# Performance work log

Measured on AMD Instinct MI355X. Metric: run time of the kernel, lower is better.

The kernel has to match this reference:

```python
import jax, jax.numpy as jnp
import numpy as np

N, F, H, F_ = 8192, 256, 2, 64
NEG_MASK = -1e10
LEAKY_SLOPE = 0.2


def setup_inputs() -> dict:
    key = jax.random.key(0)
    k0, k1, k2, k3 = jax.random.split(key, 4)
    X = jax.random.normal(k0, (N, F), jnp.float32)
    A = (jax.random.uniform(k1, (N, N)) < 0.01).astype(jnp.float32)
    A = jnp.maximum(A, jnp.eye(N, dtype=jnp.float32))
    W = jax.random.normal(k2, (H, F, F_), jnp.float32) * (1.0 / np.sqrt(F))
    b = jnp.zeros((H, F_), jnp.float32)
    a = jax.random.normal(k3, (H, F_), jnp.float32) * 0.1
    return {"X": X, "A": A, "W": W, "b": b, "a": a}


def reference(X, A, W, b, a):
    # per-head projected features: [H, N, F_]
    feats = jnp.einsum('nf,hfo->hno', X, W)
    # score[h,i,j] = sum_o feats[h,i,o] * feats[h,j,o] * a[h,o]
    # (identical math to Dot(axes=-1)([X_0*X_1, a^T]) without the [N,N,F_] tensor)
    scores = jnp.einsum('hno,hmo->hnm', feats * a[:, None, :], feats)
    scores = jax.nn.leaky_relu(scores, negative_slope=LEAKY_SLOPE)
    scores = scores + NEG_MASK * (1.0 - A)  # adjacency mask (broadcast over heads)
    attn = jax.nn.softmax(scores, axis=-1)  # [H, N, N]
    # dropout_rate=0 -> identity at inference
    out = jnp.einsum('hnm,hmo->hno', attn, feats) + b[:, None, :]  # [H, N, F_]
    out = jnp.transpose(out, (1, 0, 2)).reshape(X.shape[0], H * F_)  # concat heads
    return jax.nn.relu(out)
```

## Files before the change

kernel.cpp:

```cpp
#include <hip/hip_runtime.h>

#define NN 8192
#define FIN 256
#define FO 64
#define CAP 192

typedef float nf4 __attribute__((ext_vector_type(4)));
typedef unsigned long long ull;

__global__ __launch_bounds__(256) void feats_kernel(
    const float* __restrict__ X,
    const float* __restrict__ W,
    float* __restrict__ feats)
{
    __shared__ float Ws[128*FO];
    __shared__ float Xs[32*132];
    const int h = blockIdx.y;
    const int row0 = blockIdx.x * 32;
    const int t = threadIdx.x;
    const int rg = t >> 4;
    const int c0 = (t & 15) << 2;
    float acc0[4] = {0.f,0.f,0.f,0.f};
    float acc1[4] = {0.f,0.f,0.f,0.f};

    for (int kp = 0; kp < 2; ++kp){
        const int kb = kp * 128;
        const float* Wh = W + h*FIN*FO + kb*FO;
        #pragma unroll
        for (int it=0; it<8; ++it){
            int flat = (it*256 + t)*4;
            *(float4*)&Ws[flat] = *(const float4*)&Wh[flat];
        }
        #pragma unroll
        for (int it=0; it<4; ++it){
            int flat = (it*256 + t)*4;
            int r = flat >> 7, f0 = flat & 127;
            *(float4*)&Xs[r*132 + f0] = *(const float4*)&X[(size_t)(row0+r)*FIN + kb + f0];
        }
        __syncthreads();
        const float* xp0 = &Xs[(rg*2+0)*132];
        const float* xp1 = &Xs[(rg*2+1)*132];
        #pragma unroll 4
        for (int k=0; k<128; ++k){
            float x0 = xp0[k], x1 = xp1[k];
            float4 w4 = *(const float4*)&Ws[k*FO + c0];
            acc0[0]=fmaf(x0,w4.x,acc0[0]); acc0[1]=fmaf(x0,w4.y,acc0[1]);
            acc0[2]=fmaf(x0,w4.z,acc0[2]); acc0[3]=fmaf(x0,w4.w,acc0[3]);
            acc1[0]=fmaf(x1,w4.x,acc1[0]); acc1[1]=fmaf(x1,w4.y,acc1[1]);
            acc1[2]=fmaf(x1,w4.z,acc1[2]); acc1[3]=fmaf(x1,w4.w,acc1[3]);
        }
        __syncthreads();
    }
    float* o0 = feats + (size_t)(row0 + rg*2 + 0)*128 + h*FO + c0;
    float* o1 = feats + (size_t)(row0 + rg*2 + 1)*128 + h*FO + c0;
    *(float4*)o0 = make_float4(acc0[0],acc0[1],acc0[2],acc0[3]);
    *(float4*)o1 = make_float4(acc1[0],acc1[1],acc1[2],acc1[3]);
}

__global__ __launch_bounds__(256) void gat_kernel(
    const float* __restrict__ A,
    const float* __restrict__ feats,
    const float* __restrict__ av,
    const float* __restrict__ bv,
    float* __restrict__ out)
{
    __shared__ int   jsh[4][CAP];
    __shared__ float psh[4][2][CAP];
    __shared__ float qsh[4][128];

    const int t = threadIdx.x, w = t >> 6, l = t & 63;
    const int i = blockIdx.x*4 + w;
    const int h  = l & 1,  m  = l >> 1;
    const int ha = l >> 5, oa = (l & 31) * 2;
    const ull ltmask = (1ull << l) - 1ull;

    qsh[w][l]      = feats[(size_t)i*128 + l]      * av[l];
    qsh[w][64 + l] = feats[(size_t)i*128 + 64 + l] * av[64 + l];

    const nf4* Ar = (const nf4*)(A + (size_t)i*NN);
    int cnt = 0;
    #pragma unroll
    for (int s=0; s<4; ++s){
        nf4 v[8];
        #pragma unroll
        for (int r=0; r<8; ++r) v[r] = __builtin_nontemporal_load(&Ar[(s*8+r)*64 + l]);
        #pragma unroll
        for (int r=0; r<8; ++r){
            ull m0 = __ballot(v[r].x != 0.0f);
            ull m1 = __ballot(v[r].y != 0.0f);
            ull m2 = __ballot(v[r].z != 0.0f);
            ull m3 = __ballot(v[r].w != 0.0f);
            const int colb = ((s*8+r)*64 + l)*4;
            if ((m0>>l)&1){ int p = cnt + __popcll(m0 & ltmask); if (p<CAP) jsh[w][p] = colb;   }
            cnt += __popcll(m0);
            if ((m1>>l)&1){ int p = cnt + __popcll(m1 & ltmask); if (p<CAP) jsh[w][p] = colb+1; }
            cnt += __popcll(m1);
            if ((m2>>l)&1){ int p = cnt + __popcll(m2 & ltmask); if (p<CAP) jsh[w][p] = colb+2; }
            cnt += __popcll(m2);
            if ((m3>>l)&1){ int p = cnt + __popcll(m3 & ltmask); if (p<CAP) jsh[w][p] = colb+3; }
            cnt += __popcll(m3);
        }
    }
    const int n = min(cnt, CAP);
    __threadfence_block();

    float sr[6];
    const int nr = (n + 31) >> 5;
    float mx = -1e30f;
    const float4* qh = (const float4*)&qsh[w][h*64];
    for (int r=0; r<nr; ++r){
        int k = r*32 + m;
        bool valid = k < n;
        int j = valid ? jsh[w][k] : i;
        const float4* fj = (const float4*)&feats[(size_t)j*128 + h*64];
        float s = 0.f;
        #pragma unroll
        for (int u=0; u<16; ++u){
            float4 f = fj[u], qq = qh[u];
            s += f.x*qq.x + f.y*qq.y + f.z*qq.z + f.w*qq.w;
        }
        s = (s >= 0.f) ? s : 0.2f*s;
        if (!valid) s = -1e30f;
        sr[r] = s;
        mx = fmaxf(mx, s);
    }
    #pragma unroll
    for (int off=2; off<64; off<<=1) mx = fmaxf(mx, __shfl_xor(mx, off, 64));
    float sum = 0.f;
    for (int r=0; r<nr; ++r){ float p = __expf(sr[r] - mx); sr[r] = p; sum += p; }
    #pragma unroll
    for (int off=2; off<64; off<<=1) sum += __shfl_xor(sum, off, 64);
    const float inv = 1.0f / sum;
    for (int r=0; r<nr; ++r){
        int k = r*32 + m;
        if (k < n) psh[w][h][k] = sr[r] * inv;
    }
    __threadfence_block();

    const float* ph = psh[w][ha];
    const int fo = ha*64 + oa;
    float2 acc = make_float2(0.f, 0.f);
    int k = 0;
    for (; k+3 < n; k += 4){
        int j0 = jsh[w][k], j1 = jsh[w][k+1], j2 = jsh[w][k+2], j3 = jsh[w][k+3];
        float2 f0 = *(const float2*)&feats[(size_t)j0*128 + fo];
        float2 f1 = *(const float2*)&feats[(size_t)j1*128 + fo];
        float2 f2 = *(const float2*)&feats[(size_t)j2*128 + fo];
        float2 f3 = *(const float2*)&feats[(size_t)j3*128 + fo];
        float p0 = ph[k], p1 = ph[k+1], p2 = ph[k+2], p3 = ph[k+3];
        acc.x = fmaf(p0, f0.x, acc.x); acc.y = fmaf(p0, f0.y, acc.y);
        acc.x = fmaf(p1, f1.x, acc.x); acc.y = fmaf(p1, f1.y, acc.y);
        acc.x = fmaf(p2, f2.x, acc.x); acc.y = fmaf(p2, f2.y, acc.y);
        acc.x = fmaf(p3, f3.x, acc.x); acc.y = fmaf(p3, f3.y, acc.y);
    }
    for (; k < n; ++k){
        int j = jsh[w][k];
        float2 f = *(const float2*)&feats[(size_t)j*128 + fo];
        float p = ph[k];
        acc.x = fmaf(p, f.x, acc.x); acc.y = fmaf(p, f.y, acc.y);
    }
    float2 bb = *(const float2*)&bv[fo];
    float2 o2 = make_float2(fmaxf(acc.x + bb.x, 0.f), fmaxf(acc.y + bb.y, 0.f));
    *(float2*)&out[(size_t)i*128 + fo] = o2;
}

extern "C" void kernel_launch(void* const* d_in, const int* in_sizes, int n_in,
                              void* d_out, int out_size, void* d_ws, size_t ws_size,
                              hipStream_t stream) {
    const float* X = (const float*)d_in[0];
    const float* A = (const float*)d_in[1];
    const float* W = (const float*)d_in[2];
    const float* b = (const float*)d_in[3];
    const float* a = (const float*)d_in[4];
    float* out = (float*)d_out;

    float* feats = (float*)d_ws;

    feats_kernel<<<dim3(NN/32, 2), 256, 0, stream>>>(X, W, feats);
    gat_kernel  <<<dim3(NN/4),     256, 0, stream>>>(A, feats, a, b, out);
}
```

Measured before the change: 429.0 us.

## Double-buffer adjacency row loads and coalesce score gathers across lanes

The adjacency scan now runs eight stages of four float4 loads each, issuing the next stage's loads before the current stage is compacted. This software-pipelines the A-row stream, which dominates memory traffic, and uses fewer live registers than the previous eight-load batches. The score computation is also restructured: 16 lanes read one neighbor's 64-float head slice with coalesced float4 loads and reduce the dot product with shuffles, instead of each lane reading a whole row serially. Scores go through shared memory for a separate softmax pass, which adds a shared-memory round trip and extra shuffle reductions.

```diff
diff --git a/kernel.cpp b/kernel.cpp
--- a/kernel.cpp
+++ b/kernel.cpp
@@ -65,84 +65,101 @@
     float* __restrict__ out)
 {
     __shared__ int   jsh[4][CAP];
-    __shared__ float psh[4][2][CAP];
-    __shared__ float qsh[4][128];
+    __shared__ float sh0[4][CAP], sh1[4][CAP];
 
     const int t = threadIdx.x, w = t >> 6, l = t & 63;
     const int i = blockIdx.x*4 + w;
-    const int h  = l & 1,  m  = l >> 1;
-    const int ha = l >> 5, oa = (l & 31) * 2;
+    const int l32 = l & 31, g = l >> 5;
     const ull ltmask = (1ull << l) - 1ull;
 
-    qsh[w][l]      = feats[(size_t)i*128 + l]      * av[l];
-    qsh[w][64 + l] = feats[(size_t)i*128 + 64 + l] * av[64 + l];
+    int*   jw  = jsh[w];
+    float* sw0 = sh0[w];
+    float* sw1 = sh1[w];
+
+    float4 qa = *(const float4*)&av[l32*4];
+    float4 qf = *(const float4*)&feats[(size_t)i*128 + l32*4];
+    const float4 q4 = make_float4(qf.x*qa.x, qf.y*qa.y, qf.z*qa.z, qf.w*qa.w);
 
     const nf4* Ar = (const nf4*)(A + (size_t)i*NN);
+    nf4 cur[4], nxt[4];
+    #pragma unroll
+    for (int r=0; r<4; ++r) cur[r] = __builtin_nontemporal_load(&Ar[r*64 + l]);
     int cnt = 0;
-    #pragma unroll
-    for (int s=0; s<4; ++s){
-        nf4 v[8];
+    for (int s=0; s<8; ++s){
+        if (s < 7){
+            #pragma unroll
+            for (int r=0; r<4; ++r) nxt[r] = __builtin_nontemporal_load(&Ar[((s+1)*4+r)*64 + l]);
+        }
         #pragma unroll
-        for (int r=0; r<8; ++r) v[r] = __builtin_nontemporal_load(&Ar[(s*8+r)*64 + l]);
-        #pragma unroll
-        for (int r=0; r<8; ++r){
-            ull m0 = __ballot(v[r].x != 0.0f);
-            ull m1 = __ballot(v[r].y != 0.0f);
-            ull m2 = __ballot(v[r].z != 0.0f);
-            ull m3 = __ballot(v[r].w != 0.0f);
-            const int colb = ((s*8+r)*64 + l)*4;
-            if ((m0>>l)&1){ int p = cnt + __popcll(m0 & ltmask); if (p<CAP) jsh[w][p] = colb;   }
+        for (int r=0; r<4; ++r){
+            const int colb = ((s*4+r)*64 + l)*4;
+            bool n0 = (cur[r].x != 0.0f), n1 = (cur[r].y != 0.0f);
+            bool n2 = (cur[r].z != 0.0f), n3 = (cur[r].w != 0.0f);
+            ull m0 = __ballot(n0), m1 = __ballot(n1), m2 = __ballot(n2), m3 = __ballot(n3);
+            if (n0){ int p = cnt + __popcll(m0 & ltmask); if (p<CAP) jw[p] = colb;   }
             cnt += __popcll(m0);
-            if ((m1>>l)&1){ int p = cnt + __popcll(m1 & ltmask); if (p<CAP) jsh[w][p] = colb+1; }
+            if (n1){ int p = cnt + __popcll(m1 & ltmask); if (p<CAP) jw[p] = colb+1; }
             cnt += __popcll(m1);
-            if ((m2>>l)&1){ int p = cnt + __popcll(m2 & ltmask); if (p<CAP) jsh[w][p] = colb+2; }
+            if (n2){ int p = cnt + __popcll(m2 & ltmask); if (p<CAP) jw[p] = colb+2; }
             cnt += __popcll(m2);
-            if ((m3>>l)&1){ int p = cnt + __popcll(m3 & ltmask); if (p<CAP) jsh[w][p] = colb+3; }
+            if (n3){ int p = cnt + __popcll(m3 & ltmask); if (p<CAP) jw[p] = colb+3; }
             cnt += __popcll(m3);
         }
+        #pragma unroll
+        for (int r=0; r<4; ++r) cur[r] = nxt[r];
     }
     const int n = min(cnt, CAP);
     __threadfence_block();
 
-    float sr[6];
-    const int nr = (n + 31) >> 5;
-    float mx = -1e30f;
-    const float4* qh = (const float4*)&qsh[w][h*64];
-    for (int r=0; r<nr; ++r){
-        int k = r*32 + m;
-        bool valid = k < n;
-        int j = valid ? jsh[w][k] : i;
-        const float4* fj = (const float4*)&feats[(size_t)j*128 + h*64];
-        float s = 0.f;
+    for (int kb=0; kb<n; kb+=8){
+        float4 f[4];
         #pragma unroll
-        for (int u=0; u<16; ++u){
-            float4 f = fj[u], qq = qh[u];
-            s += f.x*qq.x + f.y*qq.y + f.z*qq.z + f.w*qq.w;
+        for (int u=0; u<4; ++u){
+            int k = kb + 2*u + g;
+            int j = (k < n) ? jw[k] : i;
+            f[u] = *(const float4*)&feats[(size_t)j*128 + l32*4];
         }
-        s = (s >= 0.f) ? s : 0.2f*s;
-        if (!valid) s = -1e30f;
-        sr[r] = s;
-        mx = fmaxf(mx, s);
-    }
-    #pragma unroll
-    for (int off=2; off<64; off<<=1) mx = fmaxf(mx, __shfl_xor(mx, off, 64));
-    float sum = 0.f;
-    for (int r=0; r<nr; ++r){ float p = __expf(sr[r] - mx); sr[r] = p; sum += p; }
-    #pragma unroll
-    for (int off=2; off<64; off<<=1) sum += __shfl_xor(sum, off, 64);
-    const float inv = 1.0f / sum;
-    for (int r=0; r<nr; ++r){
-        int k = r*32 + m;
-        if (k < n) psh[w][h][k] = sr[r] * inv;
+        #pragma unroll
+        for (int u=0; u<4; ++u){
+            int k = kb + 2*u + g;
+            float d = f[u].x*q4.x + f[u].y*q4.y + f[u].z*q4.z + f[u].w*q4.w;
+            d += __shfl_xor(d, 1, 64);
+            d += __shfl_xor(d, 2, 64);
+            d += __shfl_xor(d, 4, 64);
+            d += __shfl_xor(d, 8, 64);
+            d = (d >= 0.f) ? d : 0.2f*d;
+            if (k < n){
+                if (l32 == 0)  sw0[k] = d;
+                if (l32 == 16) sw1[k] = d;
+            }
+        }
     }
     __threadfence_block();
 
-    const float* ph = psh[w][ha];
-    const int fo = ha*64 + oa;
+    {
+        float* ss = g ? sw1 : sw0;
+        float m = -1e30f;
+        for (int k=l32; k<n; k+=32) m = fmaxf(m, ss[k]);
+        #pragma unroll
+        for (int off=16; off; off>>=1) m = fmaxf(m, __shfl_xor(m, off, 64));
+        float sum = 0.f;
+        float pr[6];
+        int nr = 0;
+        for (int k=l32; k<n; k+=32){ float p = __expf(ss[k]-m); pr[nr++] = p; sum += p; }
+        #pragma unroll
+        for (int off=16; off; off>>=1) sum += __shfl_xor(sum, off, 64);
+        const float inv = 1.0f / sum;
+        nr = 0;
+        for (int k=l32; k<n; k+=32) ss[k] = pr[nr++] * inv;
+    }
+    __threadfence_block();
+
+    const float* ph = g ? sw1 : sw0;
+    const int fo = g*64 + l32*2;
     float2 acc = make_float2(0.f, 0.f);
     int k = 0;
     for (; k+3 < n; k += 4){
-        int j0 = jsh[w][k], j1 = jsh[w][k+1], j2 = jsh[w][k+2], j3 = jsh[w][k+3];
+        int j0 = jw[k], j1 = jw[k+1], j2 = jw[k+2], j3 = jw[k+3];
         float2 f0 = *(const float2*)&feats[(size_t)j0*128 + fo];
         float2 f1 = *(const float2*)&feats[(size_t)j1*128 + fo];
         float2 f2 = *(const float2*)&feats[(size_t)j2*128 + fo];
@@ -154,7 +171,7 @@
         acc.x = fmaf(p3, f3.x, acc.x); acc.y = fmaf(p3, f3.y, acc.y);
     }
     for (; k < n; ++k){
-        int j = jsh[w][k];
+        int j = jw[k];
         float2 f = *(const float2*)&feats[(size_t)j*128 + fo];
         float p = ph[k];
         acc.x = fmaf(p, f.x, acc.x); acc.y = fmaf(p, f.y, acc.y);
```

New measurement: 392.0 us. -8.6%, faster.
